# Kernel tuning notes

Measured on AMD Instinct MI355X. Metric: run time of the kernel, lower is better.

The kernel has to match this reference:

```python
import jax, jax.numpy as jnp
import numpy as np

H = 128  # hidden/input size fixed by module


def setup_inputs() -> dict:
    key = jax.random.key(0)
    ks = jax.random.split(key, 8)
    S, B = 512, 256
    scale = 1.0 / np.sqrt(H)
    return {
        "X": jax.random.normal(ks[0], (S, B, H), dtype=jnp.float32),
        "h": jax.random.normal(ks[1], (1, B, H), dtype=jnp.float32),
        "lin_W": jax.random.uniform(ks[2], (H, H), jnp.float32, -scale, scale),
        "lin_b": jax.random.uniform(ks[3], (H,), jnp.float32, -scale, scale),
        "W_ih": jax.random.uniform(ks[4], (3 * H, H), jnp.float32, -scale, scale),
        "W_hh": jax.random.uniform(ks[5], (3 * H, H), jnp.float32, -scale, scale),
        "b_ih": jax.random.uniform(ks[6], (3 * H,), jnp.float32, -scale, scale),
        "b_hh": jax.random.uniform(ks[7], (3 * H,), jnp.float32, -scale, scale),
    }


def reference(X, h, lin_W, lin_b, W_ih, W_hh, b_ih, b_hh):
    # Linear: y = X @ W^T + b   (torch nn.Linear convention)
    Xp = jnp.einsum("sbd,ed->sbe", X, lin_W) + lin_b
    # Precompute input-hidden gate projections for all timesteps: (S, B, 3H)
    gx_all = jnp.einsum("sbd,gd->sbg", Xp, W_ih) + b_ih

    def step(h_t, gx):
        gh = h_t @ W_hh.T + b_hh  # (B, 3H)
        xr, xz, xn = jnp.split(gx, 3, axis=-1)
        hr, hz, hn = jnp.split(gh, 3, axis=-1)
        r = jax.nn.sigmoid(xr + hr)
        z = jax.nn.sigmoid(xz + hz)
        n = jnp.tanh(xn + r * hn)
        h_new = (1.0 - z) * n + z * h_t
        return h_new, h_new

    _, outs = jax.lax.scan(step, h[0], gx_all)
    return outs  # (S, B, H) — the module returns only the output sequence
```

## Files before the change

kernel.cpp:

```cpp
#include <hip/hip_runtime.h>
#include <math.h>

#define HID 128
#define G3  384
#define BATCH 256
#define SEQ 512
#define NB 16
#define NBLK (BATCH/NB)
#define NB4 4
#define NBLK4 (BATCH/NB4)

typedef __bf16 bf16x8 __attribute__((ext_vector_type(8)));
typedef __bf16 bf16x4 __attribute__((ext_vector_type(4)));
typedef float  f32x4  __attribute__((ext_vector_type(4)));

#define LOG2E 1.44269504088896f
#define SC_RZ (-1.44269504088896f)
#define SC_N  (-2.88539008177793f)

__device__ __forceinline__ float sigm(float x) {
    return __builtin_amdgcn_rcpf(1.f + __builtin_amdgcn_exp2f(-LOG2E * x));
}
__device__ __forceinline__ float tanh_fast(float x) {
    float e = __builtin_amdgcn_exp2f(-2.f * LOG2E * x);
    return __builtin_amdgcn_rcpf(1.f + e) * 2.f - 1.f;
}
__device__ __forceinline__ f32x4 mfma16(bf16x8 a, bf16x8 b, f32x4 c) {
    return __builtin_amdgcn_mfma_f32_16x16x32_bf16(a, b, c, 0, 0, 0);
}
__device__ __forceinline__ bf16x8 cvt8(float4 a, float4 b) {
    bf16x8 f;
    f[0] = (__bf16)a.x; f[1] = (__bf16)a.y; f[2] = (__bf16)a.z; f[3] = (__bf16)a.w;
    f[4] = (__bf16)b.x; f[5] = (__bf16)b.y; f[6] = (__bf16)b.z; f[7] = (__bf16)b.w;
    return f;
}
__device__ __forceinline__ bf16x8 cvt8s(float4 a, float4 b, float s) {
    bf16x8 f;
    f[0] = (__bf16)(a.x*s); f[1] = (__bf16)(a.y*s); f[2] = (__bf16)(a.z*s); f[3] = (__bf16)(a.w*s);
    f[4] = (__bf16)(b.x*s); f[5] = (__bf16)(b.y*s); f[6] = (__bf16)(b.z*s); f[7] = (__bf16)(b.w*s);
    return f;
}
__device__ __forceinline__ bf16x4 cvt4(float4 a) {
    bf16x4 f;
    f[0] = (__bf16)a.x; f[1] = (__bf16)a.y; f[2] = (__bf16)a.z; f[3] = (__bf16)a.w;
    return f;
}


__global__ void fold_bf16_kernel(const float* __restrict__ lin_W,
                                 const float* __restrict__ lin_b,
                                 const float* __restrict__ W_ih,
                                 const float* __restrict__ b_ih,
                                 __bf16* __restrict__ Wcbf,
                                 float* __restrict__ bcA) {
    const int g = blockIdx.x;
    const int d = threadIdx.x;
    const float sc = (g < 2 * HID) ? SC_RZ : SC_N;
    float acc = 0.f;
    #pragma unroll 16
    for (int e = 0; e < HID; ++e) acc += W_ih[g * HID + e] * lin_W[e * HID + d];
    Wcbf[g * HID + d] = (__bf16)(acc * sc);
    if (d == 0) {
        float b = 0.f;
        for (int e = 0; e < HID; ++e) b += W_ih[g * HID + e] * lin_b[e];
        bcA[g] = (b + b_ih[g]) * sc;
    }
}

#define GEMM_TILE(MT, CUR, NXT)                                               \
  {                                                                           \
    int mtn_ = (MT) + 1; if (mtn_ > 7) mtn_ = 7;                              \
    const float* pxn_ = X + (size_t)(m0 + mtn_ * 16 + col) * HID + lr * 8;    \
    _Pragma("unroll")                                                         \
    for (int kt = 0; kt < 4; ++kt) {                                          \
        NXT[2 * kt]     = *(const float4*)(pxn_ + kt * 32);                   \
        NXT[2 * kt + 1] = *(const float4*)(pxn_ + kt * 32 + 4);               \
    }                                                                         \
    bf16x8 Bx_[4];                                                            \
    _Pragma("unroll")                                                         \
    for (int kt = 0; kt < 4; ++kt) Bx_[kt] = cvt8(CUR[2 * kt], CUR[2 * kt + 1]); \
    const int m_ = m0 + (MT) * 16 + col;                                      \
    _Pragma("unroll")                                                         \
    for (int j = 0; j < 6; ++j) {                                             \
        f32x4 acc_ = vb[j];                                                   \
        acc_ = mfma16(A[j][0], Bx_[0], acc_);                                 \
        acc_ = mfma16(A[j][1], Bx_[1], acc_);                                 \
        acc_ = mfma16(A[j][2], Bx_[2], acc_);                                 \
        acc_ = mfma16(A[j][3], Bx_[3], acc_);                                 \
        float4 o_; o_.x = acc_[0]; o_.y = acc_[1]; o_.z = acc_[2]; o_.w = acc_[3]; \
        *(bf16x4*)(gx + (size_t)m_ * G3 + (w * 6 + j) * 16 + lr * 4) = cvt4(o_); \
    }                                                                         \
  }

__global__ __launch_bounds__(256, 2)
void gemm_gx2(const float* __restrict__ X,
              const __bf16* __restrict__ Wcbf,
              const float* __restrict__ bcA,
              __bf16* __restrict__ gx) {
    const int t   = threadIdx.x;
    const int w   = t >> 6;
    const int l   = t & 63;
    const int col = l & 15;
    const int lr  = l >> 4;
    const int m0  = blockIdx.x * 128;

    bf16x8 A[6][4];
    #pragma unroll
    for (int j = 0; j < 6; ++j)
        #pragma unroll
        for (int kt = 0; kt < 4; ++kt)
            A[j][kt] = *(const bf16x8*)(Wcbf +
                (size_t)((w * 6 + j) * 16 + col) * HID + kt * 32 + lr * 8);
    #pragma unroll
    for (int j = 0; j < 6; ++j)
        #pragma unroll
        for (int kt = 0; kt < 4; ++kt)
            asm volatile("" : "+v"(A[j][kt]));

    f32x4 vb[6];
    #pragma unroll
    for (int j = 0; j < 6; ++j)
        vb[j] = *(const f32x4*)(bcA + (w * 6 + j) * 16 + lr * 4);

    float4 xe[8], xo[8];
    {
        const float* px = X + (size_t)(m0 + col) * HID + lr * 8;
        #pragma unroll
        for (int kt = 0; kt < 4; ++kt) {
            xe[2 * kt]     = *(const float4*)(px + kt * 32);
            xe[2 * kt + 1] = *(const float4*)(px + kt * 32 + 4);
        }
    }
    for (int mt = 0; mt < 8; mt += 2) {
        GEMM_TILE(mt,     xe, xo);
        GEMM_TILE(mt + 1, xo, xe);
    }
}

#define SPLIT_STEP(S, C0, C1, C2, N0, N1, N2)                                 \
  {                                                                           \
               \
    bf16x8 Bh_[4];                                                            \
    _Pragma("unroll")                                                         \
    for (int kt = 0; kt < 4; ++kt)                                            \
        Bh_[kt] = *(const bf16x8*)(hbuf + SW(col, kt * 64 + lr * 16));        \
    f32x4 ar_ = vbr, az_ = vbz, anh_ = vbnh;                                  \
    _Pragma("unroll")                                                         \
    for (int kt = 0; kt < 4; ++kt) {                                          \
        ar_  = mfma16(aW[0][kt], Bh_[kt], ar_);                               \
        az_  = mfma16(aW[1][kt], Bh_[kt], az_);                               \
        anh_ = mfma16(aW[2][kt], Bh_[kt], anh_);                              \
    }                                                                         \
    if (col < NB4) {                                                          \
        float* gp_ = ghsF + col * 388 + w * 16 + lr * 4;                      \
        *(f32x4*)(gp_)       = ar_;                                           \
        *(f32x4*)(gp_ + 128) = az_;                                           \
        *(f32x4*)(gp_ + 256) = anh_;                                          \
    }                                                                         \
    asm volatile("s_waitcnt lgkmcnt(0)" ::: "memory");                        \
    __builtin_amdgcn_s_barrier();                                             \
                      \
    int sp_ = (S) + 1; if (sp_ > SEQ - 1) sp_ = SEQ - 1;                      \
    const __bf16* p_ = gx + (size_t)sp_ * (BATCH * G3) + gxoff;               \
    asm volatile("global_load_ushort %0, %3, off\n\t"                         \
                 "global_load_ushort %1, %3, off offset:256\n\t"              \
                 "global_load_ushort %2, %3, off offset:512"                  \
                 : "=&v"(N0), "=&v"(N1), "=&v"(N2) : "v"(p_) : "memory");     \
    float gr_ = ghsF[bi * 388 + ri];                                          \
    float gz_ = ghsF[bi * 388 + 128 + ri];                                    \
    float gn_ = ghsF[bi * 388 + 256 + ri];                                    \
                                      \
    asm volatile("s_waitcnt vmcnt(4)" ::: "memory");                          \
    __builtin_amdgcn_sched_barrier(0);                                        \
    float xr_ = __uint_as_float((C0) << 16);                                  \
    float xz_ = __uint_as_float((C1) << 16);                                  \
    float xn_ = __uint_as_float((C2) << 16);                                  \
    float r_ = __builtin_amdgcn_rcpf(1.f + __builtin_amdgcn_exp2f(gr_ + xr_));\
    float z_ = __builtin_amdgcn_rcpf(1.f + __builtin_amdgcn_exp2f(gz_ + xz_));\
    float n_ = 2.f * __builtin_amdgcn_rcpf(1.f + __builtin_amdgcn_exp2f(xn_ + r_ * gn_)) - 1.f; \
    float hn_ = n_ + z_ * (hold - n_);                                        \
    hold = hn_;                                                               \
    *(__bf16*)(hbuf + SW(bi, ri * 2)) = (__bf16)hn_;                          \
    out[((size_t)(S) * BATCH + bb + bi) * HID + ri] = hn_;                    \
    asm volatile("s_waitcnt lgkmcnt(0)" ::: "memory");                        \
    __builtin_amdgcn_s_barrier();                                             \
  }

__global__ __launch_bounds__(512, 2)
void gru_scan_split(const float* __restrict__ h0,
                    const float* __restrict__ W_hh,
                    const float* __restrict__ b_hh,
                    const __bf16* __restrict__ gx,
                    float* __restrict__ out) {
    const int t   = threadIdx.x;
    const int w   = t >> 6;
    const int l   = t & 63;
    const int col = l & 15;
    const int lr  = l >> 4;
    const int bb  = blockIdx.x * NB4;
    const int bi  = t >> 7;
    const int ri  = t & 127;

    __shared__ __align__(16) unsigned char lds[4096 + 4 * 388 * 4];
    unsigned char* hbuf = lds;
    float* ghsF = (float*)(lds + 4096);

    auto SW = [](int b, int off) { return b * 256 + (off ^ ((b & 7) << 4)); };

    bf16x8 aW[3][4];
    #pragma unroll
    for (int g3 = 0; g3 < 3; ++g3) {
        const float s = (g3 < 2) ? SC_RZ : SC_N;
        #pragma unroll
        for (int kt = 0; kt < 4; ++kt) {
            const int row = g3 * HID + w * 16 + col;
            const float* pw = W_hh + row * HID + kt * 32 + lr * 8;
            aW[g3][kt] = cvt8s(*(const float4*)pw, *(const float4*)(pw + 4), s);
        }
    }
    #pragma unroll
    for (int g3 = 0; g3 < 3; ++g3)
        #pragma unroll
        for (int kt = 0; kt < 4; ++kt)
            asm volatile("" : "+v"(aW[g3][kt]));

    f32x4 vbr, vbz, vbnh;
    #pragma unroll
    for (int q = 0; q < 4; ++q) {
        const int g = w * 16 + lr * 4 + q;
        vbr[q]  = b_hh[g] * SC_RZ;
        vbz[q]  = b_hh[HID + g] * SC_RZ;
        vbnh[q] = b_hh[2 * HID + g] * SC_N;
    }

    float hold = h0[(size_t)(bb + bi) * HID + ri];
    asm volatile("" :: "v"(hold), "v"(vbr), "v"(vbz), "v"(vbnh));

    const size_t gxoff = (size_t)(bb + bi) * G3 + ri;

    if (t < 64) {
        const int sb = t >> 4, k8 = (t & 15) * 8;
        const float* ph = h0 + (size_t)(bb + sb) * HID + k8;
        *(bf16x8*)(hbuf + SW(sb, k8 * 2)) =
            cvt8(*(const float4*)ph, *(const float4*)(ph + 4));
    } else if (t < 256) {
        const int sb = t >> 4, k8 = (t & 15) * 8;
        uint4 z = {0u, 0u, 0u, 0u};
        *(uint4*)(hbuf + SW(sb, k8 * 2)) = z;
    }

    unsigned c0, c1, c2, n0, n1, n2, dm;
    {
        const __bf16* p_ = gx + gxoff;
        asm volatile("global_load_ushort %0, %3, off\n\t"
                     "global_load_ushort %1, %3, off offset:256\n\t"
                     "global_load_ushort %2, %3, off offset:512"
                     : "=&v"(c0), "=&v"(c1), "=&v"(c2) : "v"(p_) : "memory");
        asm volatile("global_load_ushort %0, %1, off"
                     : "=&v"(dm) : "v"(p_) : "memory");
    }
    asm volatile("s_waitcnt lgkmcnt(0)" ::: "memory");
    __builtin_amdgcn_s_barrier();

    for (int s0 = 0; s0 < SEQ; s0 += 2) {
        SPLIT_STEP(s0,     c0, c1, c2, n0, n1, n2);
        SPLIT_STEP(s0 + 1, n0, n1, n2, c0, c1, c2);
    }
    asm volatile("" :: "v"(dm));
}

__global__ void fold_kernel(const float* __restrict__ lin_W,
                            const float* __restrict__ lin_b,
                            const float* __restrict__ W_ih,
                            const float* __restrict__ b_ih,
                            float* __restrict__ Wc,
                            float* __restrict__ bcA) {
    const int g = blockIdx.x;
    const int d = threadIdx.x;
    float acc = 0.f;
    for (int e = 0; e < HID; ++e) acc += W_ih[g * HID + e] * lin_W[e * HID + d];
    Wc[g * HID + d] = acc;
    if (d == 0) {
        float b = 0.f;
        for (int e = 0; e < HID; ++e) b += W_ih[g * HID + e] * lin_b[e];
        bcA[g] = b + b_ih[g];
    }
}

__global__ __launch_bounds__(512, 2)
void gru_scan_mfma(const float* __restrict__ X,
                   const float* __restrict__ h0,
                   const float* __restrict__ W_hh,
                   const float* __restrict__ b_hh,
                   const float* __restrict__ Wc,
                   const float* __restrict__ bcA,
                   float* __restrict__ out) {
    const int t   = threadIdx.x;
    const int w   = t >> 6;
    const int l   = t & 63;
    const int col = l & 15;
    const int lr  = l >> 4;
    const int bb  = blockIdx.x * NB;

    __shared__ __align__(16) unsigned char lds[16384];
    unsigned char* hA = lds;
    unsigned char* hB = lds + 4096;
    unsigned char* xA = lds + 8192;
    unsigned char* xB = lds + 12288;

    auto SW = [](int b, int off) { return b * 256 + (off ^ ((b & 7) << 4)); };

    bf16x8 aW[3][4], aC[3][4];
    #pragma unroll
    for (int g3 = 0; g3 < 3; ++g3)
        #pragma unroll
        for (int kt = 0; kt < 4; ++kt) {
            const int row = g3 * HID + w * 16 + col;
            const float* pw = W_hh + row * HID + kt * 32 + lr * 8;
            const float* pc = Wc   + row * HID + kt * 32 + lr * 8;
            aW[g3][kt] = cvt8(*(const float4*)pw, *(const float4*)(pw + 4));
            aC[g3][kt] = cvt8(*(const float4*)pc, *(const float4*)(pc + 4));
        }
    #pragma unroll
    for (int g3 = 0; g3 < 3; ++g3)
        #pragma unroll
        for (int kt = 0; kt < 4; ++kt) {
            asm volatile("" : "+v"(aW[g3][kt]));
            asm volatile("" : "+v"(aC[g3][kt]));
        }

    f32x4 vbr, vbz, vbnx, vbnh;
    #pragma unroll
    for (int q = 0; q < 4; ++q) {
        const int g = w * 16 + lr * 4 + q;
        vbr[q]  = bcA[g] + b_hh[g];
        vbz[q]  = bcA[HID + g] + b_hh[HID + g];
        vbnx[q] = bcA[2 * HID + g];
        vbnh[q] = b_hh[2 * HID + g];
    }

    f32x4 hold = *(const f32x4*)(h0 + (size_t)(bb + col) * HID + w * 16 + lr * 4);

    const int sb = t >> 5;
    const int sk = (t & 31) * 4;

    float4 xp, xq;
    if (t < 256) {
        const int hb = t >> 4, hk = (t & 15) * 8;
        const float* ph = h0 + (size_t)(bb + hb) * HID + hk;
        *(bf16x8*)(hA + SW(hb, hk * 2)) =
            cvt8(*(const float4*)ph, *(const float4*)(ph + 4));
    }
    {
        const float* px = X + ((size_t)0 * BATCH + bb + sb) * HID + sk;
        *(bf16x4*)(xA + SW(sb, sk * 2)) = cvt4(*(const float4*)px);
        const float* p1 = X + ((size_t)1 * BATCH + bb + sb) * HID + sk;
        xp = *(const float4*)p1;
    }
    asm volatile("s_waitcnt lgkmcnt(0)" ::: "memory");
    __builtin_amdgcn_s_barrier();

    auto STEP = [&](int s, unsigned char* hR, unsigned char* hW,
                    unsigned char* xR, unsigned char* xW,
                    float4& xc, float4& xn) {
        *(bf16x4*)(xW + SW(sb, sk * 2)) = cvt4(xc);
        {
            int sp = s + 2; if (sp > SEQ - 1) sp = SEQ - 1;
            const float* px = X + ((size_t)sp * BATCH + bb + sb) * HID + sk;
            xn = *(const float4*)px;
        }
        bf16x8 Bh[4], Bx[4];
        #pragma unroll
        for (int kt = 0; kt < 4; ++kt) {
            Bh[kt] = *(const bf16x8*)(hR + SW(col, kt * 64 + lr * 16));
            Bx[kt] = *(const bf16x8*)(xR + SW(col, kt * 64 + lr * 16));
        }
        f32x4 ar = vbr, az = vbz, anh = vbnh, anx = vbnx;
        #pragma unroll
        for (int kt = 0; kt < 4; ++kt) {
            ar  = mfma16(aW[0][kt], Bh[kt], ar);
            ar  = mfma16(aC[0][kt], Bx[kt], ar);
            az  = mfma16(aW[1][kt], Bh[kt], az);
            az  = mfma16(aC[1][kt], Bx[kt], az);
            anh = mfma16(aW[2][kt], Bh[kt], anh);
            anx = mfma16(aC[2][kt], Bx[kt], anx);
        }
        f32x4 hnew;
        #pragma unroll
        for (int q = 0; q < 4; ++q) {
            float r = sigm(ar[q]);
            float z = sigm(az[q]);
            float n = tanh_fast(anx[q] + r * anh[q]);
            hnew[q] = n + z * (hold[q] - n);
        }
        hold = hnew;
        *(bf16x4*)(hW + SW(col, (w * 16 + lr * 4) * 2)) = cvt4(*(float4*)&hnew);
        float4 o; o.x = hnew[0]; o.y = hnew[1]; o.z = hnew[2]; o.w = hnew[3];
        *(float4*)(out + ((size_t)s * BATCH + bb + col) * HID + w * 16 + lr * 4) = o;
        asm volatile("s_waitcnt lgkmcnt(0)" ::: "memory");
        __builtin_amdgcn_s_barrier();
    };

    for (int s0 = 0; s0 < SEQ; s0 += 2) {
        STEP(s0,     hA, hB, xA, xB, xp, xq);
        STEP(s0 + 1, hB, hA, xB, xA, xq, xp);
    }
}

extern "C" void kernel_launch(void* const* d_in, const int* in_sizes, int n_in,
                              void* d_out, int out_size, void* d_ws, size_t ws_size,
                              hipStream_t stream) {
    const float* X     = (const float*)d_in[0];
    const float* h0    = (const float*)d_in[1];
    const float* lin_W = (const float*)d_in[2];
    const float* lin_b = (const float*)d_in[3];
    const float* W_ih  = (const float*)d_in[4];
    const float* W_hh  = (const float*)d_in[5];
    const float* b_ih  = (const float*)d_in[6];
    const float* b_hh  = (const float*)d_in[7];
    float* out = (float*)d_out;

    const size_t GX_BYTES   = (size_t)SEQ * BATCH * G3 * 2;
    const size_t WCBF_BYTES = (size_t)G3 * HID * 2;
    const size_t BCA_BYTES  = (size_t)G3 * 4;

    if (ws_size >= GX_BYTES + WCBF_BYTES + BCA_BYTES) {
        __bf16* gxp  = (__bf16*)d_ws;
        __bf16* Wcbf = (__bf16*)((char*)d_ws + GX_BYTES);
        float*  bcA  = (float*)((char*)d_ws + GX_BYTES + WCBF_BYTES);

        fold_bf16_kernel<<<G3, HID, 0, stream>>>(lin_W, lin_b, W_ih, b_ih, Wcbf, bcA);
        gemm_gx2<<<(SEQ * BATCH) / 128, 256, 0, stream>>>(X, Wcbf, bcA, gxp);
        gru_scan_split<<<NBLK4, 512, 0, stream>>>(h0, W_hh, b_hh, gxp, out);
    } else {
        float* Wc  = (float*)d_ws;
        float* bcA = Wc + G3 * HID;
        fold_kernel<<<G3, HID, 0, stream>>>(lin_W, lin_b, W_ih, b_ih, Wc, bcA);
        gru_scan_mfma<<<NBLK, 512, 0, stream>>>(X, h0, W_hh, b_hh, Wc, bcA, out);
    }
}
```

Baseline: 363.7 us.

## Replace LDS gate staging with bpermute lane gather and double-buffer hidden state

The recurrent step no longer writes MFMA gate accumulators to shared memory and re-reads them after a barrier. Instead, each thread pulls its gate values directly from the owning lanes with ds_bpermute, and the thread-to-(batch,row) mapping is changed so the data stays within the wave. The hidden-state buffer is ping-ponged between two LDS halves, which removes one of the two block barriers per timestep. This costs 12 bpermutes per step plus some selects, and the next-step gx prefetch is now issued before the MFMAs.

```diff
diff --git a/kernel.cpp b/kernel.cpp
--- a/kernel.cpp
+++ b/kernel.cpp
@@ -137,13 +137,31 @@
     }
 }
 
-#define SPLIT_STEP(S, C0, C1, C2, N0, N1, N2)                                 \
+#define GATHER(V, OUT)                                                        \
   {                                                                           \
-               \
+    unsigned r0_ = (unsigned)__builtin_amdgcn_ds_bpermute(ba, (int)__float_as_uint((V)[0])); \
+    unsigned r1_ = (unsigned)__builtin_amdgcn_ds_bpermute(ba, (int)__float_as_uint((V)[1])); \
+    unsigned r2_ = (unsigned)__builtin_amdgcn_ds_bpermute(ba, (int)__float_as_uint((V)[2])); \
+    unsigned r3_ = (unsigned)__builtin_amdgcn_ds_bpermute(ba, (int)__float_as_uint((V)[3])); \
+    unsigned lo_ = q1 ? r1_ : r0_;                                            \
+    unsigned hi_ = q1 ? r3_ : r2_;                                            \
+    OUT = __uint_as_float(q2 ? hi_ : lo_);                                    \
+  }
+
+#define STEP_BP(S, HR, HW, C0, C1, C2, N0, N1, N2)                            \
+  {                                                                           \
+                            \
+    int sp_ = (S) + 1; if (sp_ > SEQ - 1) sp_ = SEQ - 1;                      \
+    const __bf16* p_ = gx + (size_t)sp_ * (BATCH * G3) + gxoff;               \
+    asm volatile("global_load_ushort %0, %3, off\n\t"                         \
+                 "global_load_ushort %1, %3, off offset:256\n\t"              \
+                 "global_load_ushort %2, %3, off offset:512"                  \
+                 : "=&v"(N0), "=&v"(N1), "=&v"(N2) : "v"(p_) : "memory");     \
+            \
     bf16x8 Bh_[4];                                                            \
     _Pragma("unroll")                                                         \
     for (int kt = 0; kt < 4; ++kt)                                            \
-        Bh_[kt] = *(const bf16x8*)(hbuf + SW(col, kt * 64 + lr * 16));        \
+        Bh_[kt] = *(const bf16x8*)((HR) + SW(col, kt * 64 + lr * 16));        \
     f32x4 ar_ = vbr, az_ = vbz, anh_ = vbnh;                                  \
     _Pragma("unroll")                                                         \
     for (int kt = 0; kt < 4; ++kt) {                                          \
@@ -151,25 +169,12 @@
         az_  = mfma16(aW[1][kt], Bh_[kt], az_);                               \
         anh_ = mfma16(aW[2][kt], Bh_[kt], anh_);                              \
     }                                                                         \
-    if (col < NB4) {                                                          \
-        float* gp_ = ghsF + col * 388 + w * 16 + lr * 4;                      \
-        *(f32x4*)(gp_)       = ar_;                                           \
-        *(f32x4*)(gp_ + 128) = az_;                                           \
-        *(f32x4*)(gp_ + 256) = anh_;                                          \
-    }                                                                         \
-    asm volatile("s_waitcnt lgkmcnt(0)" ::: "memory");                        \
-    __builtin_amdgcn_s_barrier();                                             \
-                      \
-    int sp_ = (S) + 1; if (sp_ > SEQ - 1) sp_ = SEQ - 1;                      \
-    const __bf16* p_ = gx + (size_t)sp_ * (BATCH * G3) + gxoff;               \
-    asm volatile("global_load_ushort %0, %3, off\n\t"                         \
-                 "global_load_ushort %1, %3, off offset:256\n\t"              \
-                 "global_load_ushort %2, %3, off offset:512"                  \
-                 : "=&v"(N0), "=&v"(N1), "=&v"(N2) : "v"(p_) : "memory");     \
-    float gr_ = ghsF[bi * 388 + ri];                                          \
-    float gz_ = ghsF[bi * 388 + 128 + ri];                                    \
-    float gn_ = ghsF[bi * 388 + 256 + ri];                                    \
-                                      \
+      \
+    float gr_, gz_, gn_;                                                      \
+    GATHER(ar_,  gr_);                                                        \
+    GATHER(az_,  gz_);                                                        \
+    GATHER(anh_, gn_);                                                        \
+                                               \
     asm volatile("s_waitcnt vmcnt(4)" ::: "memory");                          \
     __builtin_amdgcn_sched_barrier(0);                                        \
     float xr_ = __uint_as_float((C0) << 16);                                  \
@@ -180,32 +185,37 @@
     float n_ = 2.f * __builtin_amdgcn_rcpf(1.f + __builtin_amdgcn_exp2f(xn_ + r_ * gn_)) - 1.f; \
     float hn_ = n_ + z_ * (hold - n_);                                        \
     hold = hn_;                                                               \
-    *(__bf16*)(hbuf + SW(bi, ri * 2)) = (__bf16)hn_;                          \
+    *(__bf16*)((HW) + SW(bi, ri * 2)) = (__bf16)hn_;                          \
     out[((size_t)(S) * BATCH + bb + bi) * HID + ri] = hn_;                    \
+              \
     asm volatile("s_waitcnt lgkmcnt(0)" ::: "memory");                        \
     __builtin_amdgcn_s_barrier();                                             \
   }
 
 __global__ __launch_bounds__(512, 2)
-void gru_scan_split(const float* __restrict__ h0,
-                    const float* __restrict__ W_hh,
-                    const float* __restrict__ b_hh,
-                    const __bf16* __restrict__ gx,
-                    float* __restrict__ out) {
+void gru_scan_bp(const float* __restrict__ h0,
+                 const float* __restrict__ W_hh,
+                 const float* __restrict__ b_hh,
+                 const __bf16* __restrict__ gx,
+                 float* __restrict__ out) {
     const int t   = threadIdx.x;
     const int w   = t >> 6;
     const int l   = t & 63;
     const int col = l & 15;
     const int lr  = l >> 4;
     const int bb  = blockIdx.x * NB4;
-    const int bi  = t >> 7;
-    const int ri  = t & 127;
-
-    __shared__ __align__(16) unsigned char lds[4096 + 4 * 388 * 4];
-    unsigned char* hbuf = lds;
-    float* ghsF = (float*)(lds + 4096);
+    const int bi  = l >> 4;
+    const int ri  = w * 16 + (l & 15);
+
+    __shared__ __align__(16) unsigned char lds[8192];
+    unsigned char* hA = lds;
+    unsigned char* hB = lds + 4096;
 
     auto SW = [](int b, int off) { return b * 256 + (off ^ ((b & 7) << 4)); };
+
+    const int  ba = ((16 * ((l & 15) >> 2) + (l >> 4)) << 2);
+    const bool q1 = (l & 1) != 0;
+    const bool q2 = (l & 2) != 0;
 
     bf16x8 aW[3][4];
     #pragma unroll
@@ -238,15 +248,17 @@
 
     const size_t gxoff = (size_t)(bb + bi) * G3 + ri;
 
-    if (t < 64) {
+    if (t < 256) {
         const int sb = t >> 4, k8 = (t & 15) * 8;
-        const float* ph = h0 + (size_t)(bb + sb) * HID + k8;
-        *(bf16x8*)(hbuf + SW(sb, k8 * 2)) =
-            cvt8(*(const float4*)ph, *(const float4*)(ph + 4));
-    } else if (t < 256) {
-        const int sb = t >> 4, k8 = (t & 15) * 8;
-        uint4 z = {0u, 0u, 0u, 0u};
-        *(uint4*)(hbuf + SW(sb, k8 * 2)) = z;
+        if (sb < NB4) {
+            const float* ph = h0 + (size_t)(bb + sb) * HID + k8;
+            *(bf16x8*)(hA + SW(sb, k8 * 2)) =
+                cvt8(*(const float4*)ph, *(const float4*)(ph + 4));
+        } else {
+            uint4 z = {0u, 0u, 0u, 0u};
+            *(uint4*)(hA + SW(sb, k8 * 2)) = z;
+            *(uint4*)(hB + SW(sb, k8 * 2)) = z;
+        }
     }
 
     unsigned c0, c1, c2, n0, n1, n2, dm;
@@ -263,8 +275,8 @@
     __builtin_amdgcn_s_barrier();
 
     for (int s0 = 0; s0 < SEQ; s0 += 2) {
-        SPLIT_STEP(s0,     c0, c1, c2, n0, n1, n2);
-        SPLIT_STEP(s0 + 1, n0, n1, n2, c0, c1, c2);
+        STEP_BP(s0,     hA, hB, c0, c1, c2, n0, n1, n2);
+        STEP_BP(s0 + 1, hB, hA, n0, n1, n2, c0, c1, c2);
     }
     asm volatile("" :: "v"(dm));
 }
@@ -431,7 +443,7 @@
 
         fold_bf16_kernel<<<G3, HID, 0, stream>>>(lin_W, lin_b, W_ih, b_ih, Wcbf, bcA);
         gemm_gx2<<<(SEQ * BATCH) / 128, 256, 0, stream>>>(X, Wcbf, bcA, gxp);
-        gru_scan_split<<<NBLK4, 512, 0, stream>>>(h0, W_hh, b_hh, gxp, out);
+        gru_scan_bp<<<NBLK4, 512, 0, stream>>>(h0, W_hh, b_hh, gxp, out);
     } else {
         float* Wc  = (float*)d_ws;
         float* bcA = Wc + G3 * HID;
```

Result: no change. 369.3 us (+1.6%).

## Stage gx GEMM output through LDS for coalesced stores; pad gh LDS rows

Applied to the files above, without the earlier changes.

The input-projection GEMM used to write bf16x4 fragments straight to global memory, 8 bytes per lane spread across rows. It now stages two 16-row tiles in LDS and, after a barrier, writes full rows with coalesced 16-byte stores. It also drops the register double-buffered prefetch of X in favour of direct loads. The scan kernel's gh LDS row stride changes from 388 to 392 floats, which may change bank-conflict behaviour. In exchange, the GEMM gains two block barriers per pass and loses its explicit X prefetch overlap.

```diff
diff --git a/kernel.cpp b/kernel.cpp
--- a/kernel.cpp
+++ b/kernel.cpp
@@ -9,6 +9,7 @@
 #define NBLK (BATCH/NB)
 #define NB4 4
 #define NBLK4 (BATCH/NB4)
+#define GHP 392
 
 typedef __bf16 bf16x8 __attribute__((ext_vector_type(8)));
 typedef __bf16 bf16x4 __attribute__((ext_vector_type(4)));
@@ -67,33 +68,8 @@
     }
 }
 
-#define GEMM_TILE(MT, CUR, NXT)                                               \
-  {                                                                           \
-    int mtn_ = (MT) + 1; if (mtn_ > 7) mtn_ = 7;                              \
-    const float* pxn_ = X + (size_t)(m0 + mtn_ * 16 + col) * HID + lr * 8;    \
-    _Pragma("unroll")                                                         \
-    for (int kt = 0; kt < 4; ++kt) {                                          \
-        NXT[2 * kt]     = *(const float4*)(pxn_ + kt * 32);                   \
-        NXT[2 * kt + 1] = *(const float4*)(pxn_ + kt * 32 + 4);               \
-    }                                                                         \
-    bf16x8 Bx_[4];                                                            \
-    _Pragma("unroll")                                                         \
-    for (int kt = 0; kt < 4; ++kt) Bx_[kt] = cvt8(CUR[2 * kt], CUR[2 * kt + 1]); \
-    const int m_ = m0 + (MT) * 16 + col;                                      \
-    _Pragma("unroll")                                                         \
-    for (int j = 0; j < 6; ++j) {                                             \
-        f32x4 acc_ = vb[j];                                                   \
-        acc_ = mfma16(A[j][0], Bx_[0], acc_);                                 \
-        acc_ = mfma16(A[j][1], Bx_[1], acc_);                                 \
-        acc_ = mfma16(A[j][2], Bx_[2], acc_);                                 \
-        acc_ = mfma16(A[j][3], Bx_[3], acc_);                                 \
-        float4 o_; o_.x = acc_[0]; o_.y = acc_[1]; o_.z = acc_[2]; o_.w = acc_[3]; \
-        *(bf16x4*)(gx + (size_t)m_ * G3 + (w * 6 + j) * 16 + lr * 4) = cvt4(o_); \
-    }                                                                         \
-  }
-
 __global__ __launch_bounds__(256, 2)
-void gemm_gx2(const float* __restrict__ X,
+void gemm_gx4(const float* __restrict__ X,
               const __bf16* __restrict__ Wcbf,
               const float* __restrict__ bcA,
               __bf16* __restrict__ gx) {
@@ -104,6 +80,8 @@
     const int lr  = l >> 4;
     const int m0  = blockIdx.x * 128;
 
+    __shared__ __align__(16) unsigned char lds[32 * 784];
+
     bf16x8 A[6][4];
     #pragma unroll
     for (int j = 0; j < 6; ++j)
@@ -122,18 +100,40 @@
     for (int j = 0; j < 6; ++j)
         vb[j] = *(const f32x4*)(bcA + (w * 6 + j) * 16 + lr * 4);
 
-    float4 xe[8], xo[8];
-    {
-        const float* px = X + (size_t)(m0 + col) * HID + lr * 8;
-        #pragma unroll
-        for (int kt = 0; kt < 4; ++kt) {
-            xe[2 * kt]     = *(const float4*)(px + kt * 32);
-            xe[2 * kt + 1] = *(const float4*)(px + kt * 32 + 4);
-        }
-    }
-    for (int mt = 0; mt < 8; mt += 2) {
-        GEMM_TILE(mt,     xe, xo);
-        GEMM_TILE(mt + 1, xo, xe);
+    const int srow = t >> 3;
+    const int soff = (t & 7) * 96;
+
+    for (int p = 0; p < 4; ++p) {
+        #pragma unroll
+        for (int sub = 0; sub < 2; ++sub) {
+            const int m_ = m0 + (p * 2 + sub) * 16 + col;
+            bf16x8 Bx[4];
+            const float* px = X + (size_t)m_ * HID + lr * 8;
+            #pragma unroll
+            for (int kt = 0; kt < 4; ++kt)
+                Bx[kt] = cvt8(*(const float4*)(px + kt * 32),
+                              *(const float4*)(px + kt * 32 + 4));
+            #pragma unroll
+            for (int j = 0; j < 6; ++j) {
+                f32x4 acc = vb[j];
+                acc = mfma16(A[j][0], Bx[0], acc);
+                acc = mfma16(A[j][1], Bx[1], acc);
+                acc = mfma16(A[j][2], Bx[2], acc);
+                acc = mfma16(A[j][3], Bx[3], acc);
+                float4 o; o.x = acc[0]; o.y = acc[1]; o.z = acc[2]; o.w = acc[3];
+                *(bf16x4*)(lds + (sub * 16 + col) * 784 +
+                           ((w * 6 + j) * 16 + lr * 4) * 2) = cvt4(o);
+            }
+        }
+        __syncthreads();
+        {
+            const unsigned char* src = lds + srow * 784 + soff;
+            char* dst = (char*)gx + (size_t)(m0 + p * 32 + srow) * (G3 * 2) + soff;
+            #pragma unroll
+            for (int c = 0; c < 6; ++c)
+                *(float4*)(dst + c * 16) = *(const float4*)(src + c * 16);
+        }
+        __syncthreads();
     }
 }
 
@@ -152,7 +152,7 @@
         anh_ = mfma16(aW[2][kt], Bh_[kt], anh_);                              \
     }                                                                         \
     if (col < NB4) {                                                          \
-        float* gp_ = ghsF + col * 388 + w * 16 + lr * 4;                      \
+        float* gp_ = ghsF + col * GHP + w * 16 + lr * 4;                      \
         *(f32x4*)(gp_)       = ar_;                                           \
         *(f32x4*)(gp_ + 128) = az_;                                           \
         *(f32x4*)(gp_ + 256) = anh_;                                          \
@@ -166,9 +166,9 @@
                  "global_load_ushort %1, %3, off offset:256\n\t"              \
                  "global_load_ushort %2, %3, off offset:512"                  \
                  : "=&v"(N0), "=&v"(N1), "=&v"(N2) : "v"(p_) : "memory");     \
-    float gr_ = ghsF[bi * 388 + ri];                                          \
-    float gz_ = ghsF[bi * 388 + 128 + ri];                                    \
-    float gn_ = ghsF[bi * 388 + 256 + ri];                                    \
+    float gr_ = ghsF[bi * GHP + ri];                                          \
+    float gz_ = ghsF[bi * GHP + 128 + ri];                                    \
+    float gn_ = ghsF[bi * GHP + 256 + ri];                                    \
                                       \
     asm volatile("s_waitcnt vmcnt(4)" ::: "memory");                          \
     __builtin_amdgcn_sched_barrier(0);                                        \
@@ -201,7 +201,7 @@
     const int bi  = t >> 7;
     const int ri  = t & 127;
 
-    __shared__ __align__(16) unsigned char lds[4096 + 4 * 388 * 4];
+    __shared__ __align__(16) unsigned char lds[4096 + 4 * GHP * 4];
     unsigned char* hbuf = lds;
     float* ghsF = (float*)(lds + 4096);
 
@@ -430,7 +430,7 @@
         float*  bcA  = (float*)((char*)d_ws + GX_BYTES + WCBF_BYTES);
 
         fold_bf16_kernel<<<G3, HID, 0, stream>>>(lin_W, lin_b, W_ih, b_ih, Wcbf, bcA);
-        gemm_gx2<<<(SEQ * BATCH) / 128, 256, 0, stream>>>(X, Wcbf, bcA, gxp);
+        gemm_gx4<<<(SEQ * BATCH) / 128, 256, 0, stream>>>(X, Wcbf, bcA, gxp);
         gru_scan_split<<<NBLK4, 512, 0, stream>>>(h0, W_hh, b_hh, gxp, out);
     } else {
         float* Wc  = (float*)d_ws;
```

Result: slower. 375.2 us (+3.2%).

## Split GRU scan into 2-sequence blocks to double block count

Applied to the files above, without the earlier changes.

The recurrent scan kernel now handles 2 batch rows per block instead of 4, which doubles the grid to 128 blocks across the GPU's compute units. Only the first 256 threads do the elementwise gate update, and the LDS gate buffer padding changes to 392. The aim is to shorten the serial per-step critical path by spreading the batch over more CUs. In exchange, each block still does the full 16-column MFMA with most columns wasted, and half the threads idle during the update phase.

```diff
diff --git a/kernel.cpp b/kernel.cpp
--- a/kernel.cpp
+++ b/kernel.cpp
@@ -7,8 +7,9 @@
 #define SEQ 512
 #define NB 16
 #define NBLK (BATCH/NB)
-#define NB4 4
-#define NBLK4 (BATCH/NB4)
+#define NB2 2
+#define NBLK2 (BATCH/NB2)
+#define GHP 392
 
 typedef __bf16 bf16x8 __attribute__((ext_vector_type(8)));
 typedef __bf16 bf16x4 __attribute__((ext_vector_type(4)));
@@ -151,57 +152,59 @@
         az_  = mfma16(aW[1][kt], Bh_[kt], az_);                               \
         anh_ = mfma16(aW[2][kt], Bh_[kt], anh_);                              \
     }                                                                         \
-    if (col < NB4) {                                                          \
-        float* gp_ = ghsF + col * 388 + w * 16 + lr * 4;                      \
+    if (col < NB2) {                                                          \
+        float* gp_ = ghsF + col * GHP + w * 16 + lr * 4;                      \
         *(f32x4*)(gp_)       = ar_;                                           \
         *(f32x4*)(gp_ + 128) = az_;                                           \
         *(f32x4*)(gp_ + 256) = anh_;                                          \
     }                                                                         \
     asm volatile("s_waitcnt lgkmcnt(0)" ::: "memory");                        \
     __builtin_amdgcn_s_barrier();                                             \
-                      \
-    int sp_ = (S) + 1; if (sp_ > SEQ - 1) sp_ = SEQ - 1;                      \
-    const __bf16* p_ = gx + (size_t)sp_ * (BATCH * G3) + gxoff;               \
-    asm volatile("global_load_ushort %0, %3, off\n\t"                         \
-                 "global_load_ushort %1, %3, off offset:256\n\t"              \
-                 "global_load_ushort %2, %3, off offset:512"                  \
-                 : "=&v"(N0), "=&v"(N1), "=&v"(N2) : "v"(p_) : "memory");     \
-    float gr_ = ghsF[bi * 388 + ri];                                          \
-    float gz_ = ghsF[bi * 388 + 128 + ri];                                    \
-    float gn_ = ghsF[bi * 388 + 256 + ri];                                    \
-                                      \
-    asm volatile("s_waitcnt vmcnt(4)" ::: "memory");                          \
-    __builtin_amdgcn_sched_barrier(0);                                        \
-    float xr_ = __uint_as_float((C0) << 16);                                  \
-    float xz_ = __uint_as_float((C1) << 16);                                  \
-    float xn_ = __uint_as_float((C2) << 16);                                  \
-    float r_ = __builtin_amdgcn_rcpf(1.f + __builtin_amdgcn_exp2f(gr_ + xr_));\
-    float z_ = __builtin_amdgcn_rcpf(1.f + __builtin_amdgcn_exp2f(gz_ + xz_));\
-    float n_ = 2.f * __builtin_amdgcn_rcpf(1.f + __builtin_amdgcn_exp2f(xn_ + r_ * gn_)) - 1.f; \
-    float hn_ = n_ + z_ * (hold - n_);                                        \
-    hold = hn_;                                                               \
-    *(__bf16*)(hbuf + SW(bi, ri * 2)) = (__bf16)hn_;                          \
-    out[((size_t)(S) * BATCH + bb + bi) * HID + ri] = hn_;                    \
+                           \
+    if (t < 256) {                                                            \
+        int sp_ = (S) + 1; if (sp_ > SEQ - 1) sp_ = SEQ - 1;                  \
+        const __bf16* p_ = gx + (size_t)sp_ * (BATCH * G3) + gxoff;           \
+        asm volatile("global_load_ushort %0, %3, off\n\t"                     \
+                     "global_load_ushort %1, %3, off offset:256\n\t"          \
+                     "global_load_ushort %2, %3, off offset:512"              \
+                     : "=&v"(N0), "=&v"(N1), "=&v"(N2) : "v"(p_) : "memory"); \
+        float gr_ = ghsF[bi * GHP + ri];                                      \
+        float gz_ = ghsF[bi * GHP + 128 + ri];                                \
+        float gn_ = ghsF[bi * GHP + 256 + ri];                                \
+          \
+        asm volatile("s_waitcnt vmcnt(4)" ::: "memory");                      \
+        __builtin_amdgcn_sched_barrier(0);                                    \
+        float xr_ = __uint_as_float((C0) << 16);                              \
+        float xz_ = __uint_as_float((C1) << 16);                              \
+        float xn_ = __uint_as_float((C2) << 16);                              \
+        float r_ = __builtin_amdgcn_rcpf(1.f + __builtin_amdgcn_exp2f(gr_ + xr_)); \
+        float z_ = __builtin_amdgcn_rcpf(1.f + __builtin_amdgcn_exp2f(gz_ + xz_)); \
+        float n_ = 2.f * __builtin_amdgcn_rcpf(1.f + __builtin_amdgcn_exp2f(xn_ + r_ * gn_)) - 1.f; \
+        float hn_ = n_ + z_ * (hold - n_);                                    \
+        hold = hn_;                                                           \
+        *(__bf16*)(hbuf + SW(bi, ri * 2)) = (__bf16)hn_;                      \
+        out[((size_t)(S) * BATCH + bb + bi) * HID + ri] = hn_;                \
+    }                                                                         \
     asm volatile("s_waitcnt lgkmcnt(0)" ::: "memory");                        \
     __builtin_amdgcn_s_barrier();                                             \
   }
 
 __global__ __launch_bounds__(512, 2)
-void gru_scan_split(const float* __restrict__ h0,
-                    const float* __restrict__ W_hh,
-                    const float* __restrict__ b_hh,
-                    const __bf16* __restrict__ gx,
-                    float* __restrict__ out) {
+void gru_scan_split2(const float* __restrict__ h0,
+                     const float* __restrict__ W_hh,
+                     const float* __restrict__ b_hh,
+                     const __bf16* __restrict__ gx,
+                     float* __restrict__ out) {
     const int t   = threadIdx.x;
     const int w   = t >> 6;
     const int l   = t & 63;
     const int col = l & 15;
     const int lr  = l >> 4;
-    const int bb  = blockIdx.x * NB4;
+    const int bb  = blockIdx.x * NB2;
     const int bi  = t >> 7;
     const int ri  = t & 127;
 
-    __shared__ __align__(16) unsigned char lds[4096 + 4 * 388 * 4];
+    __shared__ __align__(16) unsigned char lds[4096 + NB2 * GHP * 4];
     unsigned char* hbuf = lds;
     float* ghsF = (float*)(lds + 4096);
 
@@ -233,12 +236,13 @@
         vbnh[q] = b_hh[2 * HID + g] * SC_N;
     }
 
-    float hold = h0[(size_t)(bb + bi) * HID + ri];
+    float hold = 0.f;
+    if (t < 256) hold = h0[(size_t)(bb + bi) * HID + ri];
     asm volatile("" :: "v"(hold), "v"(vbr), "v"(vbz), "v"(vbnh));
 
     const size_t gxoff = (size_t)(bb + bi) * G3 + ri;
 
-    if (t < 64) {
+    if (t < 32) {
         const int sb = t >> 4, k8 = (t & 15) * 8;
         const float* ph = h0 + (size_t)(bb + sb) * HID + k8;
         *(bf16x8*)(hbuf + SW(sb, k8 * 2)) =
@@ -249,8 +253,8 @@
         *(uint4*)(hbuf + SW(sb, k8 * 2)) = z;
     }
 
-    unsigned c0, c1, c2, n0, n1, n2, dm;
-    {
+    unsigned c0 = 0, c1 = 0, c2 = 0, n0, n1, n2, dm;
+    if (t < 256) {
         const __bf16* p_ = gx + gxoff;
         asm volatile("global_load_ushort %0, %3, off\n\t"
                      "global_load_ushort %1, %3, off offset:256\n\t"
@@ -266,7 +270,7 @@
         SPLIT_STEP(s0,     c0, c1, c2, n0, n1, n2);
         SPLIT_STEP(s0 + 1, n0, n1, n2, c0, c1, c2);
     }
-    asm volatile("" :: "v"(dm));
+    if (t < 256) asm volatile("" :: "v"(dm));
 }
 
 __global__ void fold_kernel(const float* __restrict__ lin_W,
@@ -431,7 +435,7 @@
 
         fold_bf16_kernel<<<G3, HID, 0, stream>>>(lin_W, lin_b, W_ih, b_ih, Wcbf, bcA);
         gemm_gx2<<<(SEQ * BATCH) / 128, 256, 0, stream>>>(X, Wcbf, bcA, gxp);
-        gru_scan_split<<<NBLK4, 512, 0, stream>>>(h0, W_hh, b_hh, gxp, out);
+        gru_scan_split2<<<NBLK2, 512, 0, stream>>>(h0, W_hh, b_hh, gxp, out);
     } else {
         float* Wc  = (float*)d_ws;
         float* bcA = Wc + G3 * HID;
```

Result: faster. 354.3 us, median of 2 (-2.6%).
